# Optimization experiments

Measured on AMD Instinct MI355X. Metric: run time of the kernel, lower is better.

## Reference

```python
import jax, jax.numpy as jnp
import numpy as np

B, T, A, D = 256, 2048, 22, 2
MAX_GAP = 512  # max NaN-gap length injected per row


def setup_inputs() -> dict:
    key = jax.random.key(0)
    k1, k2, k3 = jax.random.split(key, 3)
    x = jax.random.normal(k1, (B, T, A, D), dtype=jnp.float32)
    # one contiguous NaN gap per row: frames (s, e) exclusive are NaN
    s = jax.random.randint(k2, (B,), 1, T // 2)        # last valid frame before gap
    gap = jax.random.randint(k3, (B,), 1, MAX_GAP)     # gap length
    e = s + gap + 1                                    # first valid frame after gap
    t = jnp.arange(T)
    gap_mask = (t[None, :] > s[:, None]) & (t[None, :] < e[:, None])  # [B, T]
    x = jnp.where(gap_mask[:, :, None, None], jnp.nan, x)
    return {"x": x}


def reference(x):
    # x: [B, T, A, D] with one contiguous NaN gap along T per row.
    Bn, Tn = x.shape[0], x.shape[1]
    nan_mask = jnp.isnan(x).reshape(Bn, Tn, -1).any(axis=2)       # [B, T]
    start = jnp.argmax(nan_mask, axis=1) - 1                       # last valid before gap
    end = Tn - jnp.argmax(nan_mask[:, ::-1], axis=1)               # first valid after gap

    b = jnp.arange(Bn)
    x_s = x[b, start]                                              # [B, A, D]
    x_e = x[b, end]                                                # [B, A, D]

    t = jnp.arange(Tn)[None, :]                                    # [1, T]
    # weight at frame t is (t - s) / (e - s), matching linspace(0,1,gap+2)[1:-1]
    w = (t - start[:, None]).astype(x.dtype) / (end - start)[:, None].astype(x.dtype)
    w = w[:, :, None, None]                                        # [B, T, 1, 1]
    interp = x_s[:, None] * (1.0 - w) + x_e[:, None] * w           # [B, T, A, D]

    in_gap = (t > start[:, None]) & (t < end[:, None])             # [B, T]
    return jnp.where(in_gap[:, :, None, None], interp, x)
```

## Files before the change

### kernel.cpp

```cpp
#include <hip/hip_runtime.h>

#define BB 256
#define TT 2048
#define AD 44
#define AD4 11
#define F4_PER_B (TT * AD4)
#define ELEMS 8
#define BLK_F4 (256 * ELEMS)
#define BLOCKS_PER_B 11
#define NBLK (BB * BLOCKS_PER_B)

typedef float v4 __attribute__((ext_vector_type(4)));

__global__ __launch_bounds__(256) void scan_copy(const v4* __restrict__ x4,
                                                 v4* __restrict__ out4,
                                                 unsigned* __restrict__ mn,
                                                 unsigned* __restrict__ mxk) {
  const int tid = threadIdx.x;
  const int b = blockIdx.x / BLOCKS_PER_B;
  const int blk_in_b = blockIdx.x - b * BLOCKS_PER_B;
  const int base_in_b = blk_in_b * BLK_F4;
  const size_t base = (size_t)b * F4_PER_B + base_in_b;

  v4 v[ELEMS];
#pragma unroll
  for (int k = 0; k < ELEMS; ++k) {
    v[k] = x4[base + k * 256 + tid];
  }

  int tmin = TT;
  int tmax = -1;
#pragma unroll
  for (int k = 0; k < ELEMS; ++k) {
    const int off = k * 256 + tid;
    out4[base + off] = v[k];
    const v4 w = v[k];
    const bool n = (w.x != w.x) || (w.y != w.y) || (w.z != w.z) || (w.w != w.w);
    if (n) {
      const int t = (base_in_b + off) / AD4;
      tmin = min(tmin, t);
      tmax = max(tmax, t);
    }
  }

  const unsigned long long m = __ballot(tmax >= 0);
  if (m != 0ull) {
#pragma unroll
    for (int d = 32; d > 0; d >>= 1) {
      tmin = min(tmin, __shfl_xor(tmin, d));
      tmax = max(tmax, __shfl_xor(tmax, d));
    }
    if ((tid & 63) == 0) {
      atomicMin(&mn[b], (unsigned)tmin);
      atomicMin(&mxk[b], (unsigned)(4096 - tmax));
    }
  }
}

__global__ __launch_bounds__(256) void fix_gap(const v4* __restrict__ x4,
                                               v4* __restrict__ out4,
                                               const unsigned* __restrict__ mn,
                                               const unsigned* __restrict__ mxk) {
  const int b = blockIdx.x;
  const int tid = threadIdx.x;
  const int s = (int)mn[b] - 1;
  const int e = (4096 - (int)mxk[b]) + 1;

  __shared__ v4 sxs[AD4], sxe[AD4];
  const size_t base = (size_t)b * F4_PER_B;
  if (tid < AD4) sxs[tid] = x4[base + (size_t)s * AD4 + tid];
  if (tid >= 64 && tid < 64 + AD4) sxe[tid - 64] = x4[base + (size_t)e * AD4 + (tid - 64)];
  __syncthreads();

  const float inv = 1.0f / (float)(e - s);
  const int total = (e - s - 1) * AD4;
  for (int i = tid; i < total; i += 256) {
    const int dt = i / AD4;
    const int c = i - dt * AD4;
    const int t = s + 1 + dt;
    const float w = (float)(dt + 1) * inv;
    const float om = 1.0f - w;
    const v4 a = sxs[c];
    const v4 z = sxe[c];
    v4 r;
    r.x = a.x * om + z.x * w;
    r.y = a.y * om + z.y * w;
    r.z = a.z * om + z.z * w;
    r.w = a.w * om + z.w * w;
    out4[base + (size_t)t * AD4 + c] = r;
  }
}

extern "C" void kernel_launch(void* const* d_in, const int* in_sizes, int n_in,
                              void* d_out, int out_size, void* d_ws, size_t ws_size,
                              hipStream_t stream) {
  const v4* x4 = (const v4*)d_in[0];
  v4* out4 = (v4*)d_out;

  unsigned* mn = (unsigned*)d_ws;
  unsigned* mxk = (unsigned*)((char*)d_ws + 1024);

  hipMemsetAsync(d_ws, 0xFF, 2048, stream);

  scan_copy<<<NBLK, 256, 0, stream>>>(x4, out4, mn, mxk);
  fix_gap<<<BB, 256, 0, stream>>>(x4, out4, mn, mxk);
}
```

Before: 167.1 us.

## Fuse gap fix into scan kernel via last-block counter and nontemporal I/O

Merges the separate gap-fix kernel into the scan/copy kernel. A per-batch atomic counter elects the last finishing block to do the interpolation. The counter is initialized to 0xFFFFFFFF, so the last block sees BLOCKS_PER_B-2. Loads and stores become nontemporal, and only non-NaN vectors are written during the scan, so gap frames are not stored twice. This removes one kernel launch and the extra pass, at the cost of atomics, fences and a serialized tail per batch.

Measured after the change: 349.7 us. +109.3%, slower.

```diff
diff --git a/kernel.cpp b/kernel.cpp
--- a/kernel.cpp
+++ b/kernel.cpp
@@ -12,10 +12,11 @@
 
 typedef float v4 __attribute__((ext_vector_type(4)));
 
-__global__ __launch_bounds__(256) void scan_copy(const v4* __restrict__ x4,
-                                                 v4* __restrict__ out4,
-                                                 unsigned* __restrict__ mn,
-                                                 unsigned* __restrict__ mxk) {
+__global__ __launch_bounds__(256) void scan_fix(const v4* __restrict__ x4,
+                                                v4* __restrict__ out4,
+                                                unsigned* __restrict__ mn,
+                                                unsigned* __restrict__ mxk,
+                                                unsigned* __restrict__ cnt) {
   const int tid = threadIdx.x;
   const int b = blockIdx.x / BLOCKS_PER_B;
   const int blk_in_b = blockIdx.x - b * BLOCKS_PER_B;
@@ -25,7 +26,7 @@
   v4 v[ELEMS];
 #pragma unroll
   for (int k = 0; k < ELEMS; ++k) {
-    v[k] = x4[base + k * 256 + tid];
+    v[k] = __builtin_nontemporal_load(&x4[base + k * 256 + tid]);
   }
 
   int tmin = TT;
@@ -33,10 +34,11 @@
 #pragma unroll
   for (int k = 0; k < ELEMS; ++k) {
     const int off = k * 256 + tid;
-    out4[base + off] = v[k];
     const v4 w = v[k];
     const bool n = (w.x != w.x) || (w.y != w.y) || (w.z != w.z) || (w.w != w.w);
-    if (n) {
+    if (!n) {
+      __builtin_nontemporal_store(w, &out4[base + off]);
+    } else {
       const int t = (base_in_b + off) / AD4;
       tmin = min(tmin, t);
       tmax = max(tmax, t);
@@ -55,21 +57,35 @@
       atomicMin(&mxk[b], (unsigned)(4096 - tmax));
     }
   }
-}
 
-__global__ __launch_bounds__(256) void fix_gap(const v4* __restrict__ x4,
-                                               v4* __restrict__ out4,
-                                               const unsigned* __restrict__ mn,
-                                               const unsigned* __restrict__ mxk) {
-  const int b = blockIdx.x;
-  const int tid = threadIdx.x;
-  const int s = (int)mn[b] - 1;
-  const int e = (4096 - (int)mxk[b]) + 1;
+  __shared__ unsigned fix_flag;
+  __syncthreads();
+  if (tid == 0) {
+    __threadfence();
+    const unsigned old = atomicAdd(&cnt[b], 1u);
+    fix_flag = (old == (unsigned)(BLOCKS_PER_B - 2));
+  }
+  __syncthreads();
+  if (!fix_flag) return;
 
+  __shared__ int s_sh, e_sh;
   __shared__ v4 sxs[AD4], sxe[AD4];
-  const size_t base = (size_t)b * F4_PER_B;
-  if (tid < AD4) sxs[tid] = x4[base + (size_t)s * AD4 + tid];
-  if (tid >= 64 && tid < 64 + AD4) sxe[tid - 64] = x4[base + (size_t)e * AD4 + (tid - 64)];
+  if (tid == 0) {
+    __threadfence();
+    const unsigned mnv = __hip_atomic_load(&mn[b], __ATOMIC_ACQUIRE,
+                                           __HIP_MEMORY_SCOPE_AGENT);
+    const unsigned mxv = __hip_atomic_load(&mxk[b], __ATOMIC_ACQUIRE,
+                                           __HIP_MEMORY_SCOPE_AGENT);
+    s_sh = (int)mnv - 1;
+    e_sh = (4096 - (int)mxv) + 1;
+  }
+  __syncthreads();
+  const int s = s_sh;
+  const int e = e_sh;
+
+  const size_t bbase = (size_t)b * F4_PER_B;
+  if (tid < AD4) sxs[tid] = x4[bbase + (size_t)s * AD4 + tid];
+  if (tid >= 64 && tid < 64 + AD4) sxe[tid - 64] = x4[bbase + (size_t)e * AD4 + (tid - 64)];
   __syncthreads();
 
   const float inv = 1.0f / (float)(e - s);
@@ -87,7 +103,7 @@
     r.y = a.y * om + z.y * w;
     r.z = a.z * om + z.z * w;
     r.w = a.w * om + z.w * w;
-    out4[base + (size_t)t * AD4 + c] = r;
+    out4[bbase + (size_t)t * AD4 + c] = r;
   }
 }
 
@@ -99,9 +115,9 @@
 
   unsigned* mn = (unsigned*)d_ws;
   unsigned* mxk = (unsigned*)((char*)d_ws + 1024);
+  unsigned* cnt = (unsigned*)((char*)d_ws + 2048);
 
-  hipMemsetAsync(d_ws, 0xFF, 2048, stream);
+  hipMemsetAsync(d_ws, 0xFF, 3072, stream);
 
-  scan_copy<<<NBLK, 256, 0, stream>>>(x4, out4, mn, mxk);
-  fix_gap<<<BB, 256, 0, stream>>>(x4, out4, mn, mxk);
+  scan_fix<<<NBLK, 256, 0, stream>>>(x4, out4, mn, mxk, cnt);
 }
```

## Fuse NaN scan, copy and gap interpolation into one kernel per row

Applied to the files above, without the earlier changes.

Replaces the memset, the scan/copy kernel and the gap-fix kernel with one kernel that uses a 1024-thread block per batch row. The block loads the row in two halves, writes only non-NaN values, reduces the gap bounds through shared memory instead of global atomics, then fills the gap in the same launch. This removes two launches, the workspace memset, the atomics and the redundant stores of NaN frames. In exchange the grid shrinks to 256 large blocks, each holding many loads in flight, which may lower occupancy and load balance on a device with many CUs.

Measured after the change: 166.5 us. Within noise of the previous version (-0.3%).

```diff
diff --git a/kernel.cpp b/kernel.cpp
--- a/kernel.cpp
+++ b/kernel.cpp
@@ -2,79 +2,87 @@
 
 #define BB 256
 #define TT 2048
-#define AD 44
 #define AD4 11
 #define F4_PER_B (TT * AD4)
-#define ELEMS 8
-#define BLK_F4 (256 * ELEMS)
-#define BLOCKS_PER_B 11
-#define NBLK (BB * BLOCKS_PER_B)
+#define NTHREADS 1024
+#define HALF 11
+#define NWAVES (NTHREADS / 64)
 
 typedef float v4 __attribute__((ext_vector_type(4)));
 
-__global__ __launch_bounds__(256) void scan_copy(const v4* __restrict__ x4,
-                                                 v4* __restrict__ out4,
-                                                 unsigned* __restrict__ mn,
-                                                 unsigned* __restrict__ mxk) {
+__global__ __launch_bounds__(NTHREADS) void interp_fused(
+    const v4* __restrict__ x4, v4* __restrict__ out4) {
   const int tid = threadIdx.x;
-  const int b = blockIdx.x / BLOCKS_PER_B;
-  const int blk_in_b = blockIdx.x - b * BLOCKS_PER_B;
-  const int base_in_b = blk_in_b * BLK_F4;
-  const size_t base = (size_t)b * F4_PER_B + base_in_b;
-
-  v4 v[ELEMS];
-#pragma unroll
-  for (int k = 0; k < ELEMS; ++k) {
-    v[k] = x4[base + k * 256 + tid];
-  }
+  const int b = blockIdx.x;
+  const size_t base = (size_t)b * F4_PER_B;
 
   int tmin = TT;
   int tmax = -1;
+
 #pragma unroll
-  for (int k = 0; k < ELEMS; ++k) {
-    const int off = k * 256 + tid;
-    out4[base + off] = v[k];
-    const v4 w = v[k];
-    const bool n = (w.x != w.x) || (w.y != w.y) || (w.z != w.z) || (w.w != w.w);
-    if (n) {
-      const int t = (base_in_b + off) / AD4;
-      tmin = min(tmin, t);
-      tmax = max(tmax, t);
+  for (int h = 0; h < 2; ++h) {
+    const int hbase = h * (HALF * NTHREADS);
+    v4 v[HALF];
+#pragma unroll
+    for (int k = 0; k < HALF; ++k) {
+      v[k] = x4[base + hbase + k * NTHREADS + tid];
+    }
+#pragma unroll
+    for (int k = 0; k < HALF; ++k) {
+      const int off = hbase + k * NTHREADS + tid;
+      const v4 w = v[k];
+      const bool n = (w.x != w.x) || (w.y != w.y) || (w.z != w.z) || (w.w != w.w);
+      if (!n) {
+        out4[base + off] = w;
+      } else {
+        const int t = off / AD4;
+        tmin = min(tmin, t);
+        tmax = max(tmax, t);
+      }
     }
   }
 
-  const unsigned long long m = __ballot(tmax >= 0);
-  if (m != 0ull) {
 #pragma unroll
-    for (int d = 32; d > 0; d >>= 1) {
-      tmin = min(tmin, __shfl_xor(tmin, d));
-      tmax = max(tmax, __shfl_xor(tmax, d));
+  for (int d = 32; d > 0; d >>= 1) {
+    tmin = min(tmin, __shfl_xor(tmin, d));
+    tmax = max(tmax, __shfl_xor(tmax, d));
+  }
+
+  __shared__ int smin[NWAVES], smax[NWAVES];
+  __shared__ int s_sh, e_sh;
+  const int wid = tid >> 6;
+  if ((tid & 63) == 0) {
+    smin[wid] = tmin;
+    smax[wid] = tmax;
+  }
+  __syncthreads();
+  if (tid == 0) {
+    int a = TT, z = -1;
+#pragma unroll
+    for (int i = 0; i < NWAVES; ++i) {
+      a = min(a, smin[i]);
+      z = max(z, smax[i]);
     }
-    if ((tid & 63) == 0) {
-      atomicMin(&mn[b], (unsigned)tmin);
-      atomicMin(&mxk[b], (unsigned)(4096 - tmax));
+    if (z < 0) {
+      s_sh = 0;
+      e_sh = 1;
+    } else {
+      s_sh = a - 1;
+      e_sh = z + 1;
     }
   }
-}
-
-__global__ __launch_bounds__(256) void fix_gap(const v4* __restrict__ x4,
-                                               v4* __restrict__ out4,
-                                               const unsigned* __restrict__ mn,
-                                               const unsigned* __restrict__ mxk) {
-  const int b = blockIdx.x;
-  const int tid = threadIdx.x;
-  const int s = (int)mn[b] - 1;
-  const int e = (4096 - (int)mxk[b]) + 1;
+  __syncthreads();
+  const int s = s_sh;
+  const int e = e_sh;
 
   __shared__ v4 sxs[AD4], sxe[AD4];
-  const size_t base = (size_t)b * F4_PER_B;
   if (tid < AD4) sxs[tid] = x4[base + (size_t)s * AD4 + tid];
   if (tid >= 64 && tid < 64 + AD4) sxe[tid - 64] = x4[base + (size_t)e * AD4 + (tid - 64)];
   __syncthreads();
 
   const float inv = 1.0f / (float)(e - s);
   const int total = (e - s - 1) * AD4;
-  for (int i = tid; i < total; i += 256) {
+  for (int i = tid; i < total; i += NTHREADS) {
     const int dt = i / AD4;
     const int c = i - dt * AD4;
     const int t = s + 1 + dt;
@@ -96,12 +104,5 @@
                               hipStream_t stream) {
   const v4* x4 = (const v4*)d_in[0];
   v4* out4 = (v4*)d_out;
-
-  unsigned* mn = (unsigned*)d_ws;
-  unsigned* mxk = (unsigned*)((char*)d_ws + 1024);
-
-  hipMemsetAsync(d_ws, 0xFF, 2048, stream);
-
-  scan_copy<<<NBLK, 256, 0, stream>>>(x4, out4, mn, mxk);
-  fix_gap<<<BB, 256, 0, stream>>>(x4, out4, mn, mxk);
+  interp_fused<<<BB, NTHREADS, 0, stream>>>(x4, out4);
 }
```
